# Optimization experiments

Hardware: AMD Instinct MI355X
Metric: run time of the kernel (lower is better)

## Reference

```python
import jax, jax.numpy as jnp
import numpy as np

N, E, DIN, DH, H, B = 50000, 800000, 128, 32, 8, 512
NEG_SLOPE = 0.2


def glorot(key, shape):
    fan_in, fan_out = shape[0], shape[-1]
    lim = (6.0 / (fan_in + fan_out)) ** 0.5
    return jax.random.uniform(key, shape, jnp.float32, -lim, lim)


def setup_inputs() -> dict:
    key = jax.random.key(0)
    ks = jax.random.split(key, 16)
    x = jax.random.normal(ks[0], (N, DIN), jnp.float32)
    edge_index = jax.random.randint(ks[1], (2, E), 0, N, jnp.int64)
    batch = jnp.sort(jax.random.randint(ks[2], (N,), 0, B, jnp.int64))
    edge_weight = jax.random.uniform(ks[3], (E, 1), jnp.float32)
    # layer 1: GATv2Conv(DIN -> DH, heads=H, edge_dim=1)
    Wl1 = glorot(ks[4], (DIN, H * DH))
    Wr1 = glorot(ks[5], (DIN, H * DH))
    We1 = glorot(ks[6], (1, H * DH))
    att1 = glorot(ks[7], (H, DH))
    b1 = jnp.zeros((H * DH,), jnp.float32)
    # layer 2: GATv2Conv(H*DH -> DH, heads=1, edge_dim=1)
    Wl2 = glorot(ks[8], (H * DH, DH))
    Wr2 = glorot(ks[9], (H * DH, DH))
    We2 = glorot(ks[10], (1, DH))
    att2 = glorot(ks[11], (1, DH))
    b2 = jnp.zeros((DH,), jnp.float32)
    Wfc = glorot(ks[12], (DH, 1))
    bfc = jnp.zeros((1,), jnp.float32)
    return dict(x=x, edge_index=edge_index, batch=batch, edge_weight=edge_weight,
                Wl1=Wl1, Wr1=Wr1, We1=We1, att1=att1, b1=b1,
                Wl2=Wl2, Wr2=Wr2, We2=We2, att2=att2, b2=b2,
                Wfc=Wfc, bfc=bfc)


def gatv2_layer(x, src, dst, ew, Wl, Wr, We, att, bias, heads, out_ch):
    n = x.shape[0]
    xl = (x @ Wl).reshape(n, heads, out_ch)   # source transform
    xr = (x @ Wr).reshape(n, heads, out_ch)   # target transform
    ee = (ew @ We).reshape(-1, heads, out_ch)  # edge attr transform
    z = xl[src] + xr[dst] + ee                 # [E,H,C]
    s = jnp.einsum('ehc,hc->eh', jax.nn.leaky_relu(z, NEG_SLOPE), att)
    # segment softmax over edges sharing the same target node
    m = jax.ops.segment_max(s, dst, num_segments=n)
    ex = jnp.exp(s - m[dst])
    den = jax.ops.segment_sum(ex, dst, num_segments=n)
    alpha = ex / (den[dst] + 1e-16)            # [E,H]
    out = jax.ops.segment_sum(alpha[..., None] * xl[src], dst, num_segments=n)
    return out.reshape(n, heads * out_ch) + bias


def add_self_loops(edge_index, edge_weight, n):
    loops = jnp.arange(n, dtype=edge_index.dtype)
    src = jnp.concatenate([edge_index[0], loops])
    dst = jnp.concatenate([edge_index[1], loops])
    fill = jnp.mean(edge_weight, axis=0, keepdims=True)  # fill_value='mean'
    ew = jnp.concatenate([edge_weight, jnp.broadcast_to(fill, (n, edge_weight.shape[1]))])
    return src, dst, ew


def reference(x, edge_index, batch, edge_weight,
              Wl1, Wr1, We1, att1, b1,
              Wl2, Wr2, We2, att2, b2,
              Wfc, bfc):
    n = x.shape[0]
    src, dst, ew = add_self_loops(edge_index, edge_weight, n)
    h = gatv2_layer(x, src, dst, ew, Wl1, Wr1, We1, att1, b1, H, DH)
    h = jax.nn.relu(h)
    h = gatv2_layer(h, src, dst, ew, Wl2, Wr2, We2, att2, b2, 1, DH)
    feat = jax.nn.relu(h)
    # global mean pool over graphs
    sums = jax.ops.segment_sum(feat, batch, num_segments=B)
    cnt = jax.ops.segment_sum(jnp.ones((n, 1), feat.dtype), batch, num_segments=B)
    feat = sums / jnp.maximum(cnt, 1.0)
    feat = jax.nn.sigmoid(feat)
    return feat @ Wfc + bfc  # [B,1]
```

## Files before the change

### kernel.cpp

```cpp
#include <hip/hip_runtime.h>
#include <math.h>

#define N_NODES 50000
#define N_EDGES 800000
#define D_IN    128
#define D_H     32
#define N_HEADS 8
#define N_GRAPHS 512
#define E_TOT   (N_EDGES + N_NODES)
#define HDIM    (N_HEADS * D_H)
#define NEG_SLOPE 0.2f
#define NSCAN_BLK ((N_NODES + 255) / 256)
#define LOG2E 1.4426950408889634f
#define RESCALE_THR2 11.0f

typedef short bfrag8 __attribute__((ext_vector_type(8)));
typedef float f32x4 __attribute__((ext_vector_type(4)));
typedef float f32x2 __attribute__((ext_vector_type(2)));

#if __has_builtin(__builtin_amdgcn_exp2f)
#define EXP2(x) __builtin_amdgcn_exp2f(x)
#else
#define EXP2(x) exp2f(x)
#endif

__device__ __forceinline__ unsigned short f2b(float x) {
    unsigned u = __float_as_uint(x);
    unsigned r = u + 0x7FFFu + ((u >> 16) & 1u);
    return (unsigned short)(r >> 16);
}
__device__ __forceinline__ f32x2 b2x2(unsigned u) {
    f32x2 v;
    v.x = __uint_as_float(u << 16);
    v.y = __uint_as_float(u & 0xFFFF0000u);
    return v;
}

__device__ __forceinline__ float dpp8_sum(float x) {
    x += __int_as_float(__builtin_amdgcn_mov_dpp(__float_as_int(x), 0xB1, 0xF, 0xF, true));
    x += __int_as_float(__builtin_amdgcn_mov_dpp(__float_as_int(x), 0x4E, 0xF, 0xF, true));
    x += __int_as_float(__builtin_amdgcn_mov_dpp(__float_as_int(x), 0x141, 0xF, 0xF, true));
    return x;
}

#define RS_BLK   512
#define HIST_BLK ((E_TOT + 255) / 256)
#define W1_BLK   (512 * 128 / 256)
#define W2_BLK   (64 * 256 / 256)
__global__ void k_front(const float* __restrict__ ew, const int* __restrict__ ei,
                        const float* __restrict__ Wl1, const float* __restrict__ Wr1,
                        const float* __restrict__ Wl2, const float* __restrict__ Wr2,
                        float* __restrict__ fillsum, int* __restrict__ deg,
                        unsigned short* __restrict__ Wt1,
                        unsigned short* __restrict__ Wt2) {
    __shared__ float ls[4];
    int b = blockIdx.x;
    if (b < RS_BLK) {
        int t = b * 256 + threadIdx.x;
        float s = 0.f;
        for (int i = t; i < N_EDGES; i += RS_BLK * 256) s += ew[i];
        for (int m = 1; m < 64; m <<= 1) s += __shfl_xor(s, m);
        int lane = threadIdx.x & 63, wv = threadIdx.x >> 6;
        if (lane == 0) ls[wv] = s;
        __syncthreads();
        if (threadIdx.x == 0) atomicAdd(fillsum, ls[0] + ls[1] + ls[2] + ls[3]);
    } else if (b < RS_BLK + HIST_BLK) {
        int e = (b - RS_BLK) * 256 + threadIdx.x;
        if (e >= E_TOT) return;
        int dst = (e < N_EDGES) ? ei[N_EDGES + e] : (e - N_EDGES);
        atomicAdd(&deg[dst], 1);
    } else if (b < RS_BLK + HIST_BLK + W1_BLK) {
        int t = (b - RS_BLK - HIST_BLK) * 256 + threadIdx.x;
        int c = t >> 7, k = t & 127;
        float v = (c < 256) ? Wl1[k * 256 + c] : Wr1[k * 256 + (c - 256)];
        Wt1[t] = f2b(v);
    } else {
        int t = (b - RS_BLK - HIST_BLK - W1_BLK) * 256 + threadIdx.x;
        int c = t >> 8, k = t & 255;
        float v = (c < 32) ? Wl2[k * 32 + c] : Wr2[k * 32 + (c - 32)];
        Wt2[t] = f2b(v);
    }
}

__global__ void k_scan1(const int* __restrict__ deg, int* __restrict__ start,
                        int* __restrict__ bsum) {
    __shared__ int sh[256];
    int i = blockIdx.x * 256 + threadIdx.x;
    int v = (i < N_NODES) ? deg[i] : 0;
    sh[threadIdx.x] = v;
    __syncthreads();
    for (int o = 1; o < 256; o <<= 1) {
        int t = (threadIdx.x >= o) ? sh[threadIdx.x - o] : 0;
        __syncthreads();
        sh[threadIdx.x] += t;
        __syncthreads();
    }
    if (i < N_NODES) start[i] = sh[threadIdx.x] - v;
    if (threadIdx.x == 255) bsum[blockIdx.x] = sh[255];
}
__global__ void k_scan2(int* __restrict__ bsum, int nb) {
    __shared__ int sh[256];
    int v = (threadIdx.x < nb) ? bsum[threadIdx.x] : 0;
    sh[threadIdx.x] = v;
    __syncthreads();
    for (int o = 1; o < 256; o <<= 1) {
        int t = (threadIdx.x >= o) ? sh[threadIdx.x - o] : 0;
        __syncthreads();
        sh[threadIdx.x] += t;
        __syncthreads();
    }
    if (threadIdx.x < nb) bsum[threadIdx.x] = sh[threadIdx.x] - v;
}
__global__ void k_scan3(int* __restrict__ start, const int* __restrict__ bsum,
                        int* __restrict__ cur) {
    int i = blockIdx.x * 256 + threadIdx.x;
    if (i < N_NODES) {
        int v = start[i] + bsum[blockIdx.x];
        start[i] = v;
        cur[i] = v;
    }
}

__global__ void k_scatter(const int* __restrict__ ei, const float* __restrict__ ew,
                          const float* __restrict__ fillsum,
                          int* __restrict__ cur, int2* __restrict__ csr) {
    int e = blockIdx.x * blockDim.x + threadIdx.x;
    if (e >= E_TOT) return;
    int src, dst; float w;
    if (e < N_EDGES) { src = ei[e]; dst = ei[N_EDGES + e]; w = ew[e]; }
    else { src = dst = e - N_EDGES; w = fillsum[0] * (1.0f / N_EDGES); }
    int pos = atomicAdd(&cur[dst], 1);
    csr[pos] = make_int2(src, __float_as_int(w));
}

__global__ __launch_bounds__(256) void k_gemm1(
    const float* __restrict__ A, const unsigned short* __restrict__ Bt,
    unsigned short* __restrict__ C, int M)
{
    const int KC = 128, NN = 512;
    __shared__ unsigned short A_lds[128][KC + 8];
    __shared__ unsigned short B_lds[128][KC + 8];
    int row0 = blockIdx.y * 128, col0 = blockIdx.x * 128;
    int tid = threadIdx.x;
    for (int idx = tid; idx < 128 * 32; idx += 256) {
        int r = idx >> 5, c4 = idx & 31;
        int gr = row0 + r;
        float4 v = {0.f, 0.f, 0.f, 0.f};
        if (gr < M) v = ((const float4*)(A + (size_t)gr * KC))[c4];
        ushort4 o;
        o.x = f2b(v.x); o.y = f2b(v.y); o.z = f2b(v.z); o.w = f2b(v.w);
        *(ushort4*)&A_lds[r][c4 * 4] = o;
    }
    for (int idx = tid; idx < 128 * 16; idx += 256) {
        int r = idx >> 4, ch = idx & 15;
        uint4 v = *(const uint4*)(Bt + (size_t)(col0 + r) * KC + ch * 8);
        *(uint4*)&B_lds[r][ch * 8] = v;
    }
    __syncthreads();

    int wid = tid >> 6, lane = tid & 63;
    int wy = wid >> 1, wx = wid & 1;
    int lr = lane & 15, lh = lane >> 4;
    f32x4 acc[4][4] = {};
    #pragma unroll
    for (int k0 = 0; k0 < KC; k0 += 32) {
        bfrag8 af[4], bf[4];
        #pragma unroll
        for (int i = 0; i < 4; ++i) {
            af[i] = *(const bfrag8*)&A_lds[64 * wy + 16 * i + lr][k0 + lh * 8];
            bf[i] = *(const bfrag8*)&B_lds[64 * wx + 16 * i + lr][k0 + lh * 8];
        }
        #pragma unroll
        for (int mi = 0; mi < 4; ++mi)
            #pragma unroll
            for (int ni = 0; ni < 4; ++ni)
                acc[mi][ni] = __builtin_amdgcn_mfma_f32_16x16x32_bf16(af[mi], bf[ni], acc[mi][ni], 0, 0, 0);
    }
    #pragma unroll
    for (int mi = 0; mi < 4; ++mi) {
        #pragma unroll
        for (int ni = 0; ni < 4; ++ni) {
            #pragma unroll
            for (int r = 0; r < 4; ++r) {
                int row = row0 + 64 * wy + 16 * mi + lh * 4 + r;
                if (row < M)
                    C[(size_t)row * NN + col0 + 64 * wx + 16 * ni + lr] = f2b(acc[mi][ni][r]);
            }
        }
    }
}

__global__ __launch_bounds__(256) void k_gemm2(
    const unsigned short* __restrict__ A, const unsigned short* __restrict__ Bt,
    unsigned short* __restrict__ C, int M)
{
    const int KC = 256, NN = 64;
    __shared__ unsigned short A_lds[64][KC + 8];
    __shared__ unsigned short B_lds[64][KC + 8];
    int row0 = blockIdx.y * 64, col0 = 0;
    int tid = threadIdx.x;
    const int CPR = KC / 8;
    for (int idx = tid; idx < 64 * CPR; idx += 256) {
        int r = idx / CPR, ch = idx % CPR;
        int gr = row0 + r;
        uint4 v = {0u, 0u, 0u, 0u};
        if (gr < M) v = *(const uint4*)(A + (size_t)gr * KC + ch * 8);
        *(uint4*)&A_lds[r][ch * 8] = v;
    }
    for (int idx = tid; idx < 64 * CPR; idx += 256) {
        int r = idx / CPR, ch = idx % CPR;
        uint4 v = *(const uint4*)(Bt + (size_t)(col0 + r) * KC + ch * 8);
        *(uint4*)&B_lds[r][ch * 8] = v;
    }
    __syncthreads();

    int wid = tid >> 6, lane = tid & 63;
    int wy = wid >> 1, wx = wid & 1;
    int lr = lane & 15, lh = lane >> 4;
    f32x4 acc[2][2] = {};
    #pragma unroll
    for (int k0 = 0; k0 < KC; k0 += 32) {
        bfrag8 a0 = *(const bfrag8*)&A_lds[32 * wy + lr][k0 + lh * 8];
        bfrag8 a1 = *(const bfrag8*)&A_lds[32 * wy + 16 + lr][k0 + lh * 8];
        bfrag8 b0 = *(const bfrag8*)&B_lds[32 * wx + lr][k0 + lh * 8];
        bfrag8 b1 = *(const bfrag8*)&B_lds[32 * wx + 16 + lr][k0 + lh * 8];
        acc[0][0] = __builtin_amdgcn_mfma_f32_16x16x32_bf16(a0, b0, acc[0][0], 0, 0, 0);
        acc[0][1] = __builtin_amdgcn_mfma_f32_16x16x32_bf16(a0, b1, acc[0][1], 0, 0, 0);
        acc[1][0] = __builtin_amdgcn_mfma_f32_16x16x32_bf16(a1, b0, acc[1][0], 0, 0, 0);
        acc[1][1] = __builtin_amdgcn_mfma_f32_16x16x32_bf16(a1, b1, acc[1][1], 0, 0, 0);
    }
    #pragma unroll
    for (int mt = 0; mt < 2; ++mt) {
        #pragma unroll
        for (int nt = 0; nt < 2; ++nt) {
            #pragma unroll
            for (int r = 0; r < 4; ++r) {
                int row = row0 + 32 * wy + 16 * mt + lh * 4 + r;
                if (row < M)
                    C[(size_t)row * NN + col0 + 32 * wx + 16 * nt + lr] = f2b(acc[mt][nt][r]);
            }
        }
    }
}

__global__ __launch_bounds__(256) void k_gat1(
    const unsigned short* __restrict__ xlr,
    const int* __restrict__ start, const int* __restrict__ deg,
    const int2* __restrict__ csr,
    const float* __restrict__ We, const float* __restrict__ att,
    const float* __restrict__ b1, unsigned short* __restrict__ out1)
{
    int wid = (blockIdx.x * blockDim.x + threadIdx.x) >> 6;
    int lane = threadIdx.x & 63;
    if (wid >= N_NODES) return;
    f32x2 we01 = ((const f32x2*)We)[2 * lane],  we23 = ((const f32x2*)We)[2 * lane + 1];
    f32x2 at01 = ((const f32x2*)att)[2 * lane], at23 = ((const f32x2*)att)[2 * lane + 1];
    at01 *= LOG2E; at23 *= LOG2E;
    uint2 xru = *(const uint2*)(xlr + (size_t)wid * 512 + 256 + 4 * lane);
    f32x2 xr01 = b2x2(xru.x), xr23 = b2x2(xru.y);
    int s0 = start[wid], dg = deg[wid];
    const int2* ep = csr + s0;
    float m = -1e30f, d = 0.f;
    f32x2 acc01 = {0.f, 0.f}, acc23 = {0.f, 0.f};

    int dmax = dg - 1;
    int2 e0 = ep[0];
    int2 e1 = ep[1 < dmax ? 1 : dmax];
    int2 e2 = ep[2 < dmax ? 2 : dmax];
    int2 e3 = ep[3 < dmax ? 3 : dmax];
    uint2 r0 = *(const uint2*)(xlr + ((size_t)e0.x << 9) + 4 * lane);
    uint2 r1 = *(const uint2*)(xlr + ((size_t)e1.x << 9) + 4 * lane);
    uint2 r2 = *(const uint2*)(xlr + ((size_t)e2.x << 9) + 4 * lane);
    uint2 r3 = *(const uint2*)(xlr + ((size_t)e3.x << 9) + 4 * lane);

    for (int j = 0; j < dg; j += 4) {
        float w0 = __int_as_float(e0.y), w1 = __int_as_float(e1.y);
        float w2 = __int_as_float(e2.y), w3 = __int_as_float(e3.y);
        f32x2 a001 = b2x2(r0.x), a023 = b2x2(r0.y);
        f32x2 a101 = b2x2(r1.x), a123 = b2x2(r1.y);
        f32x2 a201 = b2x2(r2.x), a223 = b2x2(r2.y);
        f32x2 a301 = b2x2(r3.x), a323 = b2x2(r3.y);
        int jn = j + 4;
        if (jn < dg) {
            e0 = ep[jn];
            e1 = ep[jn + 1 < dmax ? jn + 1 : dmax];
            e2 = ep[jn + 2 < dmax ? jn + 2 : dmax];
            e3 = ep[jn + 3 < dmax ? jn + 3 : dmax];
            r0 = *(const uint2*)(xlr + ((size_t)e0.x << 9) + 4 * lane);
            r1 = *(const uint2*)(xlr + ((size_t)e1.x << 9) + 4 * lane);
            r2 = *(const uint2*)(xlr + ((size_t)e2.x << 9) + 4 * lane);
            r3 = *(const uint2*)(xlr + ((size_t)e3.x << 9) + 4 * lane);
        }
        f32x2 z, lz, ww, pv;
        ww = (f32x2){w0, w0}; pv = (f32x2){0.f, 0.f};
        z = a001 + __builtin_elementwise_fma(ww, we01, xr01);
        lz = __builtin_elementwise_max(z, z * NEG_SLOPE);
        pv = __builtin_elementwise_fma(lz, at01, pv);
        z = a023 + __builtin_elementwise_fma(ww, we23, xr23);
        lz = __builtin_elementwise_max(z, z * NEG_SLOPE);
        pv = __builtin_elementwise_fma(lz, at23, pv);
        float p0 = pv.x + pv.y;
        ww = (f32x2){w1, w1}; pv = (f32x2){0.f, 0.f};
        z = a101 + __builtin_elementwise_fma(ww, we01, xr01);
        lz = __builtin_elementwise_max(z, z * NEG_SLOPE);
        pv = __builtin_elementwise_fma(lz, at01, pv);
        z = a123 + __builtin_elementwise_fma(ww, we23, xr23);
        lz = __builtin_elementwise_max(z, z * NEG_SLOPE);
        pv = __builtin_elementwise_fma(lz, at23, pv);
        float p1 = pv.x + pv.y;
        ww = (f32x2){w2, w2}; pv = (f32x2){0.f, 0.f};
        z = a201 + __builtin_elementwise_fma(ww, we01, xr01);
        lz = __builtin_elementwise_max(z, z * NEG_SLOPE);
        pv = __builtin_elementwise_fma(lz, at01, pv);
        z = a223 + __builtin_elementwise_fma(ww, we23, xr23);
        lz = __builtin_elementwise_max(z, z * NEG_SLOPE);
        pv = __builtin_elementwise_fma(lz, at23, pv);
        float p2 = pv.x + pv.y;
        ww = (f32x2){w3, w3}; pv = (f32x2){0.f, 0.f};
        z = a301 + __builtin_elementwise_fma(ww, we01, xr01);
        lz = __builtin_elementwise_max(z, z * NEG_SLOPE);
        pv = __builtin_elementwise_fma(lz, at01, pv);
        z = a323 + __builtin_elementwise_fma(ww, we23, xr23);
        lz = __builtin_elementwise_max(z, z * NEG_SLOPE);
        pv = __builtin_elementwise_fma(lz, at23, pv);
        float p3 = pv.x + pv.y;
        p0 = dpp8_sum(p0); p1 = dpp8_sum(p1);
        p2 = dpp8_sum(p2); p3 = dpp8_sum(p3);
        if (j + 1 >= dg) p1 = -1e30f;
        if (j + 2 >= dg) p2 = -1e30f;
        if (j + 3 >= dg) p3 = -1e30f;
        float pm = fmaxf(fmaxf(p0, p1), fmaxf(p2, p3));
        if (__any(pm > m + RESCALE_THR2)) {
            float nm = fmaxf(m, pm);
            float sc = EXP2(m - nm);
            d *= sc;
            acc01 *= sc; acc23 *= sc;
            m = nm;
        }
        float q0 = EXP2(p0 - m), q1 = EXP2(p1 - m);
        float q2 = EXP2(p2 - m), q3 = EXP2(p3 - m);
        d += (q0 + q1) + (q2 + q3);
        f32x2 qq;
        qq = (f32x2){q0, q0};
        acc01 = __builtin_elementwise_fma(qq, a001, acc01);
        acc23 = __builtin_elementwise_fma(qq, a023, acc23);
        qq = (f32x2){q1, q1};
        acc01 = __builtin_elementwise_fma(qq, a101, acc01);
        acc23 = __builtin_elementwise_fma(qq, a123, acc23);
        qq = (f32x2){q2, q2};
        acc01 = __builtin_elementwise_fma(qq, a201, acc01);
        acc23 = __builtin_elementwise_fma(qq, a223, acc23);
        qq = (f32x2){q3, q3};
        acc01 = __builtin_elementwise_fma(qq, a301, acc01);
        acc23 = __builtin_elementwise_fma(qq, a323, acc23);
    }
    float inv = 1.f / (d + 1e-16f);
    f32x2 b01 = ((const f32x2*)b1)[2 * lane], b23 = ((const f32x2*)b1)[2 * lane + 1];
    ushort4 o;
    o.x = f2b(fmaxf(fmaf(acc01.x, inv, b01.x), 0.f));
    o.y = f2b(fmaxf(fmaf(acc01.y, inv, b01.y), 0.f));
    o.z = f2b(fmaxf(fmaf(acc23.x, inv, b23.x), 0.f));
    o.w = f2b(fmaxf(fmaf(acc23.y, inv, b23.y), 0.f));
    *(ushort4*)(out1 + (size_t)wid * 256 + 4 * lane) = o;
}

__global__ __launch_bounds__(256) void k_gat2(
    const unsigned short* __restrict__ xlr2,
    const int* __restrict__ start, const int* __restrict__ deg,
    const int2* __restrict__ csr,
    const float* __restrict__ We, const float* __restrict__ att,
    const float* __restrict__ b2, const int* __restrict__ batch,
    float* __restrict__ pool, float* __restrict__ cnt)
{
    int gt = blockIdx.x * blockDim.x + threadIdx.x;
    int i = gt >> 3, g = gt & 7;
    if (i >= N_NODES) return;
    f32x2 we01 = ((const f32x2*)We)[2 * g],  we23 = ((const f32x2*)We)[2 * g + 1];
    f32x2 at01 = ((const f32x2*)att)[2 * g], at23 = ((const f32x2*)att)[2 * g + 1];
    at01 *= LOG2E; at23 *= LOG2E;
    uint2 xru = *(const uint2*)(xlr2 + (size_t)i * 64 + 32 + 4 * g);
    f32x2 xr01 = b2x2(xru.x), xr23 = b2x2(xru.y);
    int s0 = start[i], dg = deg[i];
    const int2* ep = csr + s0;
    float m = -1e30f, d = 0.f;
    f32x2 acc01 = {0.f, 0.f}, acc23 = {0.f, 0.f};

    int dmax = dg - 1;
    int2 e0 = ep[0];
    int2 e1 = ep[1 < dmax ? 1 : dmax];
    int2 e2 = ep[2 < dmax ? 2 : dmax];
    int2 e3 = ep[3 < dmax ? 3 : dmax];
    uint2 r0 = *(const uint2*)(xlr2 + ((size_t)e0.x << 6) + 4 * g);
    uint2 r1 = *(const uint2*)(xlr2 + ((size_t)e1.x << 6) + 4 * g);
    uint2 r2 = *(const uint2*)(xlr2 + ((size_t)e2.x << 6) + 4 * g);
    uint2 r3 = *(const uint2*)(xlr2 + ((size_t)e3.x << 6) + 4 * g);

    for (int j = 0; j < dg; j += 4) {
        float w0 = __int_as_float(e0.y), w1 = __int_as_float(e1.y);
        float w2 = __int_as_float(e2.y), w3 = __int_as_float(e3.y);
        f32x2 a001 = b2x2(r0.x), a023 = b2x2(r0.y);
        f32x2 a101 = b2x2(r1.x), a123 = b2x2(r1.y);
        f32x2 a201 = b2x2(r2.x), a223 = b2x2(r2.y);
        f32x2 a301 = b2x2(r3.x), a323 = b2x2(r3.y);
        int jn = j + 4;
        if (jn < dg) {
            e0 = ep[jn];
            e1 = ep[jn + 1 < dmax ? jn + 1 : dmax];
            e2 = ep[jn + 2 < dmax ? jn + 2 : dmax];
            e3 = ep[jn + 3 < dmax ? jn + 3 : dmax];
            r0 = *(const uint2*)(xlr2 + ((size_t)e0.x << 6) + 4 * g);
            r1 = *(const uint2*)(xlr2 + ((size_t)e1.x << 6) + 4 * g);
            r2 = *(const uint2*)(xlr2 + ((size_t)e2.x << 6) + 4 * g);
            r3 = *(const uint2*)(xlr2 + ((size_t)e3.x << 6) + 4 * g);
        }
        f32x2 z, lz, ww, pv;
        ww = (f32x2){w0, w0}; pv = (f32x2){0.f, 0.f};
        z = a001 + __builtin_elementwise_fma(ww, we01, xr01);
        lz = __builtin_elementwise_max(z, z * NEG_SLOPE);
        pv = __builtin_elementwise_fma(lz, at01, pv);
        z = a023 + __builtin_elementwise_fma(ww, we23, xr23);
        lz = __builtin_elementwise_max(z, z * NEG_SLOPE);
        pv = __builtin_elementwise_fma(lz, at23, pv);
        float p0 = pv.x + pv.y;
        ww = (f32x2){w1, w1}; pv = (f32x2){0.f, 0.f};
        z = a101 + __builtin_elementwise_fma(ww, we01, xr01);
        lz = __builtin_elementwise_max(z, z * NEG_SLOPE);
        pv = __builtin_elementwise_fma(lz, at01, pv);
        z = a123 + __builtin_elementwise_fma(ww, we23, xr23);
        lz = __builtin_elementwise_max(z, z * NEG_SLOPE);
        pv = __builtin_elementwise_fma(lz, at23, pv);
        float p1 = pv.x + pv.y;
        ww = (f32x2){w2, w2}; pv = (f32x2){0.f, 0.f};
        z = a201 + __builtin_elementwise_fma(ww, we01, xr01);
        lz = __builtin_elementwise_max(z, z * NEG_SLOPE);
        pv = __builtin_elementwise_fma(lz, at01, pv);
        z = a223 + __builtin_elementwise_fma(ww, we23, xr23);
        lz = __builtin_elementwise_max(z, z * NEG_SLOPE);
        pv = __builtin_elementwise_fma(lz, at23, pv);
        float p2 = pv.x + pv.y;
        ww = (f32x2){w3, w3}; pv = (f32x2){0.f, 0.f};
        z = a301 + __builtin_elementwise_fma(ww, we01, xr01);
        lz = __builtin_elementwise_max(z, z * NEG_SLOPE);
        pv = __builtin_elementwise_fma(lz, at01, pv);
        z = a323 + __builtin_elementwise_fma(ww, we23, xr23);
        lz = __builtin_elementwise_max(z, z * NEG_SLOPE);
        pv = __builtin_elementwise_fma(lz, at23, pv);
        float p3 = pv.x + pv.y;
        p0 = dpp8_sum(p0); p1 = dpp8_sum(p1);
        p2 = dpp8_sum(p2); p3 = dpp8_sum(p3);
        if (j + 1 >= dg) p1 = -1e30f;
        if (j + 2 >= dg) p2 = -1e30f;
        if (j + 3 >= dg) p3 = -1e30f;
        float pm = fmaxf(fmaxf(p0, p1), fmaxf(p2, p3));
        if (__any(pm > m + RESCALE_THR2)) {
            float nm = fmaxf(m, pm);
            float sc = EXP2(m - nm);
            d *= sc;
            acc01 *= sc; acc23 *= sc;
            m = nm;
        }
        float q0 = EXP2(p0 - m), q1 = EXP2(p1 - m);
        float q2 = EXP2(p2 - m), q3 = EXP2(p3 - m);
        d += (q0 + q1) + (q2 + q3);
        f32x2 qq;
        qq = (f32x2){q0, q0};
        acc01 = __builtin_elementwise_fma(qq, a001, acc01);
        acc23 = __builtin_elementwise_fma(qq, a023, acc23);
        qq = (f32x2){q1, q1};
        acc01 = __builtin_elementwise_fma(qq, a101, acc01);
        acc23 = __builtin_elementwise_fma(qq, a123, acc23);
        qq = (f32x2){q2, q2};
        acc01 = __builtin_elementwise_fma(qq, a201, acc01);
        acc23 = __builtin_elementwise_fma(qq, a223, acc23);
        qq = (f32x2){q3, q3};
        acc01 = __builtin_elementwise_fma(qq, a301, acc01);
        acc23 = __builtin_elementwise_fma(qq, a323, acc23);
    }
    float inv = 1.f / (d + 1e-16f);
    f32x2 b01 = ((const f32x2*)b2)[2 * g], b23 = ((const f32x2*)b2)[2 * g + 1];
    float vx = fmaxf(fmaf(acc01.x, inv, b01.x), 0.f);
    float vy = fmaxf(fmaf(acc01.y, inv, b01.y), 0.f);
    float vz = fmaxf(fmaf(acc23.x, inv, b23.x), 0.f);
    float vw = fmaxf(fmaf(acc23.y, inv, b23.y), 0.f);
    int b = batch[i];
    float* o = pool + (size_t)b * D_H + g * 4;
    atomicAdd(o + 0, vx);
    atomicAdd(o + 1, vy);
    atomicAdd(o + 2, vz);
    atomicAdd(o + 3, vw);
    if (g == 0) atomicAdd(&cnt[b], 1.0f);
}

__global__ void k_final(const float* __restrict__ pool, const float* __restrict__ cnt,
                        const float* __restrict__ Wfc, const float* __restrict__ bfc,
                        float* __restrict__ out)
{
    int b = blockIdx.x * blockDim.x + threadIdx.x;
    if (b >= N_GRAPHS) return;
    float c = cnt[b]; c = c > 1.f ? c : 1.f;
    float acc = 0.f;
    #pragma unroll
    for (int j = 0; j < D_H; ++j) {
        float f = pool[b * D_H + j] / c;
        f = 1.f / (1.f + __expf(-f));
        acc = fmaf(f, Wfc[j], acc);
    }
    out[b] = acc + bfc[0];
}

extern "C" void kernel_launch(void* const* d_in, const int* in_sizes, int n_in,
                              void* d_out, int out_size, void* d_ws, size_t ws_size,
                              hipStream_t stream)
{
    const float* x    = (const float*)d_in[0];
    const int*   ei   = (const int*)  d_in[1];
    const int*   batch= (const int*)  d_in[2];
    const float* ew   = (const float*)d_in[3];
    const float* Wl1  = (const float*)d_in[4];
    const float* Wr1  = (const float*)d_in[5];
    const float* We1  = (const float*)d_in[6];
    const float* att1 = (const float*)d_in[7];
    const float* b1   = (const float*)d_in[8];
    const float* Wl2  = (const float*)d_in[9];
    const float* Wr2  = (const float*)d_in[10];
    const float* We2  = (const float*)d_in[11];
    const float* att2 = (const float*)d_in[12];
    const float* b2   = (const float*)d_in[13];
    const float* Wfc  = (const float*)d_in[14];
    const float* bfc  = (const float*)d_in[15];
    float* out = (float*)d_out;

    float* ws = (float*)d_ws;
    size_t off = 0;
    auto take = [&](size_t n) -> float* {
        float* p = ws + off;
        off = (off + n + 63) & ~(size_t)63;
        return p;
    };
    float* fillsum = take(1);
    int*   deg  = (int*)take(N_NODES);
    float* cnt  = take(N_GRAPHS);
    float* pool = take((size_t)N_GRAPHS * D_H);
    size_t zero_elems = off;
    int*   start = (int*)take(N_NODES);
    int*   cur   = (int*)take(N_NODES);
    int*   bsum  = (int*)take(256);
    int2*  csr   = (int2*)take((size_t)E_TOT * 2);
    unsigned short* Wt1  = (unsigned short*)take(512 * 128 / 2);
    unsigned short* Wt2  = (unsigned short*)take(64 * 256 / 2);
    unsigned short* xlr1 = (unsigned short*)take((size_t)N_NODES * 512 / 2);
    unsigned short* out1 = (unsigned short*)take((size_t)N_NODES * 256 / 2);
    unsigned short* xlr2 = (unsigned short*)take((size_t)N_NODES * 64 / 2);
    (void)ws_size; (void)in_sizes; (void)n_in; (void)out_size;

    hipMemsetAsync(d_ws, 0, zero_elems * sizeof(float), stream);

    k_front<<<RS_BLK + HIST_BLK + W1_BLK + W2_BLK, 256, 0, stream>>>(
        ew, ei, Wl1, Wr1, Wl2, Wr2, fillsum, deg, Wt1, Wt2);

    k_scan1<<<NSCAN_BLK, 256, 0, stream>>>(deg, start, bsum);
    k_scan2<<<1, 256, 0, stream>>>(bsum, NSCAN_BLK);
    k_scan3<<<NSCAN_BLK, 256, 0, stream>>>(start, bsum, cur);
    k_scatter<<<(E_TOT + 255) / 256, 256, 0, stream>>>(ei, ew, fillsum, cur, csr);

    k_gemm1<<<dim3(512 / 128, (N_NODES + 127) / 128), 256, 0, stream>>>(
        x, Wt1, xlr1, N_NODES);

    k_gat1<<<(N_NODES * 64 + 255) / 256, 256, 0, stream>>>(
        xlr1, start, deg, csr, We1, att1, b1, out1);

    k_gemm2<<<dim3(1, (N_NODES + 63) / 64), 256, 0, stream>>>(
        out1, Wt2, xlr2, N_NODES);

    k_gat2<<<((size_t)N_NODES * 8 + 255) / 256, 256, 0, stream>>>(
        xlr2, start, deg, csr, We2, att2, b2, batch, pool, cnt);

    k_final<<<(N_GRAPHS + 255) / 256, 256, 0, stream>>>(pool, cnt, Wfc, bfc, out);
}
```

Before: 334.7 us.

## Split layer-2 GAT edges across eight lane groups per node with online-softmax merge

Layer-2 attention now gives each node a full 64-lane wavefront instead of 8 lanes. Eight sub-groups each take every eighth incoming edge and keep their own online softmax state. The partial max, denominator and accumulators are then merged with xor shuffles. This shortens the per-node serial edge loop and exposes more parallel gathers for latency hiding, at the cost of 8x more threads, idle lanes for low-degree nodes (average degree is about 17), and the shuffle-merge overhead.

```diff
diff --git a/kernel.cpp b/kernel.cpp
--- a/kernel.cpp
+++ b/kernel.cpp
@@ -372,123 +372,91 @@
     const float* __restrict__ b2, const int* __restrict__ batch,
     float* __restrict__ pool, float* __restrict__ cnt)
 {
-    int gt = blockIdx.x * blockDim.x + threadIdx.x;
-    int i = gt >> 3, g = gt & 7;
+    int i = (blockIdx.x * blockDim.x + threadIdx.x) >> 6;
+    int lane = threadIdx.x & 63;
     if (i >= N_NODES) return;
-    f32x2 we01 = ((const f32x2*)We)[2 * g],  we23 = ((const f32x2*)We)[2 * g + 1];
-    f32x2 at01 = ((const f32x2*)att)[2 * g], at23 = ((const f32x2*)att)[2 * g + 1];
+    int s = lane >> 3;
+    int c = lane & 7;
+    f32x2 we01 = ((const f32x2*)We)[2 * c],  we23 = ((const f32x2*)We)[2 * c + 1];
+    f32x2 at01 = ((const f32x2*)att)[2 * c], at23 = ((const f32x2*)att)[2 * c + 1];
     at01 *= LOG2E; at23 *= LOG2E;
-    uint2 xru = *(const uint2*)(xlr2 + (size_t)i * 64 + 32 + 4 * g);
+    uint2 xru = *(const uint2*)(xlr2 + (size_t)i * 64 + 32 + 4 * c);
     f32x2 xr01 = b2x2(xru.x), xr23 = b2x2(xru.y);
     int s0 = start[i], dg = deg[i];
     const int2* ep = csr + s0;
     float m = -1e30f, d = 0.f;
     f32x2 acc01 = {0.f, 0.f}, acc23 = {0.f, 0.f};
 
-    int dmax = dg - 1;
-    int2 e0 = ep[0];
-    int2 e1 = ep[1 < dmax ? 1 : dmax];
-    int2 e2 = ep[2 < dmax ? 2 : dmax];
-    int2 e3 = ep[3 < dmax ? 3 : dmax];
-    uint2 r0 = *(const uint2*)(xlr2 + ((size_t)e0.x << 6) + 4 * g);
-    uint2 r1 = *(const uint2*)(xlr2 + ((size_t)e1.x << 6) + 4 * g);
-    uint2 r2 = *(const uint2*)(xlr2 + ((size_t)e2.x << 6) + 4 * g);
-    uint2 r3 = *(const uint2*)(xlr2 + ((size_t)e3.x << 6) + 4 * g);
-
-    for (int j = 0; j < dg; j += 4) {
-        float w0 = __int_as_float(e0.y), w1 = __int_as_float(e1.y);
-        float w2 = __int_as_float(e2.y), w3 = __int_as_float(e3.y);
-        f32x2 a001 = b2x2(r0.x), a023 = b2x2(r0.y);
-        f32x2 a101 = b2x2(r1.x), a123 = b2x2(r1.y);
-        f32x2 a201 = b2x2(r2.x), a223 = b2x2(r2.y);
-        f32x2 a301 = b2x2(r3.x), a323 = b2x2(r3.y);
-        int jn = j + 4;
-        if (jn < dg) {
-            e0 = ep[jn];
-            e1 = ep[jn + 1 < dmax ? jn + 1 : dmax];
-            e2 = ep[jn + 2 < dmax ? jn + 2 : dmax];
-            e3 = ep[jn + 3 < dmax ? jn + 3 : dmax];
-            r0 = *(const uint2*)(xlr2 + ((size_t)e0.x << 6) + 4 * g);
-            r1 = *(const uint2*)(xlr2 + ((size_t)e1.x << 6) + 4 * g);
-            r2 = *(const uint2*)(xlr2 + ((size_t)e2.x << 6) + 4 * g);
-            r3 = *(const uint2*)(xlr2 + ((size_t)e3.x << 6) + 4 * g);
-        }
-        f32x2 z, lz, ww, pv;
-        ww = (f32x2){w0, w0}; pv = (f32x2){0.f, 0.f};
-        z = a001 + __builtin_elementwise_fma(ww, we01, xr01);
+    int T = (dg + 7) >> 3;
+    int j0 = s < dg ? s : dg - 1;
+    int2 e = ep[j0];
+    uint2 r = *(const uint2*)(xlr2 + ((size_t)e.x << 6) + 4 * c);
+
+    for (int t = 0; t < T; ++t) {
+        bool valid = (t * 8 + s) < dg;
+        int2 ce = e; uint2 cr = r;
+        if (t + 1 < T) {
+            int jn = (t + 1) * 8 + s;
+            if (jn >= dg) jn = dg - 1;
+            e = ep[jn];
+            r = *(const uint2*)(xlr2 + ((size_t)e.x << 6) + 4 * c);
+        }
+        float w = __int_as_float(ce.y);
+        f32x2 a01 = b2x2(cr.x), a23 = b2x2(cr.y);
+        f32x2 ww = {w, w}, pv = {0.f, 0.f}, z, lz;
+        z = a01 + __builtin_elementwise_fma(ww, we01, xr01);
         lz = __builtin_elementwise_max(z, z * NEG_SLOPE);
         pv = __builtin_elementwise_fma(lz, at01, pv);
-        z = a023 + __builtin_elementwise_fma(ww, we23, xr23);
+        z = a23 + __builtin_elementwise_fma(ww, we23, xr23);
         lz = __builtin_elementwise_max(z, z * NEG_SLOPE);
         pv = __builtin_elementwise_fma(lz, at23, pv);
-        float p0 = pv.x + pv.y;
-        ww = (f32x2){w1, w1}; pv = (f32x2){0.f, 0.f};
-        z = a101 + __builtin_elementwise_fma(ww, we01, xr01);
-        lz = __builtin_elementwise_max(z, z * NEG_SLOPE);
-        pv = __builtin_elementwise_fma(lz, at01, pv);
-        z = a123 + __builtin_elementwise_fma(ww, we23, xr23);
-        lz = __builtin_elementwise_max(z, z * NEG_SLOPE);
-        pv = __builtin_elementwise_fma(lz, at23, pv);
-        float p1 = pv.x + pv.y;
-        ww = (f32x2){w2, w2}; pv = (f32x2){0.f, 0.f};
-        z = a201 + __builtin_elementwise_fma(ww, we01, xr01);
-        lz = __builtin_elementwise_max(z, z * NEG_SLOPE);
-        pv = __builtin_elementwise_fma(lz, at01, pv);
-        z = a223 + __builtin_elementwise_fma(ww, we23, xr23);
-        lz = __builtin_elementwise_max(z, z * NEG_SLOPE);
-        pv = __builtin_elementwise_fma(lz, at23, pv);
-        float p2 = pv.x + pv.y;
-        ww = (f32x2){w3, w3}; pv = (f32x2){0.f, 0.f};
-        z = a301 + __builtin_elementwise_fma(ww, we01, xr01);
-        lz = __builtin_elementwise_max(z, z * NEG_SLOPE);
-        pv = __builtin_elementwise_fma(lz, at01, pv);
-        z = a323 + __builtin_elementwise_fma(ww, we23, xr23);
-        lz = __builtin_elementwise_max(z, z * NEG_SLOPE);
-        pv = __builtin_elementwise_fma(lz, at23, pv);
-        float p3 = pv.x + pv.y;
-        p0 = dpp8_sum(p0); p1 = dpp8_sum(p1);
-        p2 = dpp8_sum(p2); p3 = dpp8_sum(p3);
-        if (j + 1 >= dg) p1 = -1e30f;
-        if (j + 2 >= dg) p2 = -1e30f;
-        if (j + 3 >= dg) p3 = -1e30f;
-        float pm = fmaxf(fmaxf(p0, p1), fmaxf(p2, p3));
-        if (__any(pm > m + RESCALE_THR2)) {
-            float nm = fmaxf(m, pm);
+        float p = dpp8_sum(pv.x + pv.y);
+        if (!valid) p = -1e30f;
+        if (__any(p > m + RESCALE_THR2)) {
+            float nm = fmaxf(m, p);
             float sc = EXP2(m - nm);
             d *= sc;
             acc01 *= sc; acc23 *= sc;
             m = nm;
         }
-        float q0 = EXP2(p0 - m), q1 = EXP2(p1 - m);
-        float q2 = EXP2(p2 - m), q3 = EXP2(p3 - m);
-        d += (q0 + q1) + (q2 + q3);
-        f32x2 qq;
-        qq = (f32x2){q0, q0};
-        acc01 = __builtin_elementwise_fma(qq, a001, acc01);
-        acc23 = __builtin_elementwise_fma(qq, a023, acc23);
-        qq = (f32x2){q1, q1};
-        acc01 = __builtin_elementwise_fma(qq, a101, acc01);
-        acc23 = __builtin_elementwise_fma(qq, a123, acc23);
-        qq = (f32x2){q2, q2};
-        acc01 = __builtin_elementwise_fma(qq, a201, acc01);
-        acc23 = __builtin_elementwise_fma(qq, a223, acc23);
-        qq = (f32x2){q3, q3};
-        acc01 = __builtin_elementwise_fma(qq, a301, acc01);
-        acc23 = __builtin_elementwise_fma(qq, a323, acc23);
-    }
-    float inv = 1.f / (d + 1e-16f);
-    f32x2 b01 = ((const f32x2*)b2)[2 * g], b23 = ((const f32x2*)b2)[2 * g + 1];
-    float vx = fmaxf(fmaf(acc01.x, inv, b01.x), 0.f);
-    float vy = fmaxf(fmaf(acc01.y, inv, b01.y), 0.f);
-    float vz = fmaxf(fmaf(acc23.x, inv, b23.x), 0.f);
-    float vw = fmaxf(fmaf(acc23.y, inv, b23.y), 0.f);
-    int b = batch[i];
-    float* o = pool + (size_t)b * D_H + g * 4;
-    atomicAdd(o + 0, vx);
-    atomicAdd(o + 1, vy);
-    atomicAdd(o + 2, vz);
-    atomicAdd(o + 3, vw);
-    if (g == 0) atomicAdd(&cnt[b], 1.0f);
+        float q = valid ? EXP2(p - m) : 0.f;
+        d += q;
+        f32x2 qq = {q, q};
+        acc01 = __builtin_elementwise_fma(qq, a01, acc01);
+        acc23 = __builtin_elementwise_fma(qq, a23, acc23);
+    }
+
+    #pragma unroll
+    for (int off = 8; off <= 32; off <<= 1) {
+        float mo = __shfl_xor(m, off);
+        float dd = __shfl_xor(d, off);
+        f32x2 ao01, ao23;
+        ao01.x = __shfl_xor(acc01.x, off); ao01.y = __shfl_xor(acc01.y, off);
+        ao23.x = __shfl_xor(acc23.x, off); ao23.y = __shfl_xor(acc23.y, off);
+        float nm = fmaxf(m, mo);
+        float sa = EXP2(m - nm), sb = EXP2(mo - nm);
+        d = d * sa + dd * sb;
+        f32x2 va = {sa, sa}, vb = {sb, sb};
+        acc01 = acc01 * va + ao01 * vb;
+        acc23 = acc23 * va + ao23 * vb;
+        m = nm;
+    }
+
+    if (s == 0) {
+        float inv = 1.f / (d + 1e-16f);
+        f32x2 b01 = ((const f32x2*)b2)[2 * c], b23 = ((const f32x2*)b2)[2 * c + 1];
+        float vx = fmaxf(fmaf(acc01.x, inv, b01.x), 0.f);
+        float vy = fmaxf(fmaf(acc01.y, inv, b01.y), 0.f);
+        float vz = fmaxf(fmaf(acc23.x, inv, b23.x), 0.f);
+        float vw = fmaxf(fmaf(acc23.y, inv, b23.y), 0.f);
+        int b = batch[i];
+        float* o = pool + (size_t)b * D_H + c * 4;
+        atomicAdd(o + 0, vx);
+        atomicAdd(o + 1, vy);
+        atomicAdd(o + 2, vz);
+        atomicAdd(o + 3, vw);
+        if (c == 0) atomicAdd(&cnt[b], 1.0f);
+    }
 }
 
 __global__ void k_final(const float* __restrict__ pool, const float* __restrict__ cnt,
@@ -572,7 +540,7 @@
     k_gemm2<<<dim3(1, (N_NODES + 63) / 64), 256, 0, stream>>>(
         out1, Wt2, xlr2, N_NODES);
 
-    k_gat2<<<((size_t)N_NODES * 8 + 255) / 256, 256, 0, stream>>>(
+    k_gat2<<<((size_t)N_NODES * 64 + 255) / 256, 256, 0, stream>>>(
         xlr2, start, deg, csr, We2, att2, b2, batch, pool, cnt);
 
     k_final<<<(N_GRAPHS + 255) / 256, 256, 0, stream>>>(pool, cnt, Wfc, bfc, out);
```

New measurement: 368.8 us. 1.1x slower.
